# Optimization experiments

Measured on AMD Instinct MI355X. Metric: run time of the kernel, lower is better.

Reference implementation:

```python
import jax, jax.numpy as jnp
import numpy as np

NUM_ROWS = 16384
H = 2048
K = 4
EXPERT_NUM = 64


def setup_inputs() -> dict:
    key = jax.random.key(0)
    k1, k2, k3 = jax.random.split(key, 3)
    x = jax.random.normal(k1, (NUM_ROWS, H), dtype=jnp.float32)
    expert_idx = jax.random.randint(k2, (NUM_ROWS, K), 0, EXPERT_NUM, dtype=jnp.int32)
    scale = jax.random.uniform(k3, (NUM_ROWS,), dtype=jnp.float32)
    return {"x": x, "expert_idx": expert_idx, "scale": scale, "expert_num": EXPERT_NUM}


def reference(x, expert_idx, scale, expert_num):
    # Dropless MoE token routing (drop_pad_mode=0, active_num=0 -> all tokens,
    # quant_mode=-1 with scale, expert_tokens_num_type=1, full active range).
    num_rows, h = x.shape
    k = expert_idx.shape[-1]
    n = num_rows * k
    eidx = expert_idx.reshape(-1)                     # [n]
    sorted_idx = jnp.argsort(eidx, stable=True)       # stable sort by expert id
    src_row = sorted_idx // k                         # original token row per expanded slot
    expanded_x = x[src_row]                           # [n, h] gathered tokens, expert-grouped
    # inverse permutation: position of each original (row,k) slot in the expanded output
    expanded_row_idx = jnp.zeros((n,), dtype=jnp.int32).at[sorted_idx].set(
        jnp.arange(n, dtype=jnp.int32))
    expert_tokens_count = jnp.bincount(eidx, length=expert_num).astype(jnp.int32)
    expanded_scale = scale[src_row].astype(jnp.float32)  # [n]
    return expanded_x, expanded_row_idx, expert_tokens_count, expanded_scale
```

## Files before the change

### kernel.cpp

```cpp
#include <hip/hip_runtime.h>

#define NROWS   16384
#define HDIM    2048
#define TOPK    4
#define NEXP    64
#define NSLOT   (NROWS * TOPK)
#define SLOTS_PER_BLOCK 256
#define NBLK    (NSLOT / SLOTS_PER_BLOCK)
#define CHUNK   16
#define NCHUNK  (NBLK / CHUNK)

typedef float f4 __attribute__((ext_vector_type(4)));

__global__ void hist_rank_kernel(const int* __restrict__ eidx,
                                 int* __restrict__ hist,
                                 int* __restrict__ packed) {
    __shared__ int se[SLOTS_PER_BLOCK];
    __shared__ int h[NEXP];
    int t = threadIdx.x;
    if (t < NEXP) h[t] = 0;
    int slot = blockIdx.x * SLOTS_PER_BLOCK + t;
    int e = eidx[slot];
    se[t] = e;
    __syncthreads();
    int rank = 0, cnt = 0;
    #pragma unroll 8
    for (int i = 0; i < SLOTS_PER_BLOCK; ++i) {
        int m = (se[i] == e);
        cnt  += m;
        rank += (i < t) ? m : 0;
    }
    packed[slot] = (e << 16) | rank;
    if (rank == 0) h[e] = cnt;
    __syncthreads();
    if (t < NEXP) hist[blockIdx.x * NEXP + t] = h[t];
}

__global__ void __launch_bounds__(1024) scan_kernel(const int* __restrict__ hist,
                                                    int* __restrict__ base,
                                                    float* __restrict__ out_counts) {
    __shared__ int partial[NCHUNK][NEXP];
    __shared__ int expert_off[NEXP];
    int tid = threadIdx.x;
    int c = tid >> 6;
    int e = tid & 63;
    int b0 = c * CHUNK;

    int s = 0;
    #pragma unroll
    for (int i = 0; i < CHUNK; ++i) s += hist[(b0 + i) * NEXP + e];
    partial[c][e] = s;
    __syncthreads();

    int excl = 0;
    #pragma unroll
    for (int i = 0; i < NCHUNK; ++i) {
        int v = partial[i][e];
        excl += (i < c) ? v : 0;
    }

    if (tid < 64) {
        int total = 0;
        #pragma unroll
        for (int i = 0; i < NCHUNK; ++i) total += partial[i][tid];
        out_counts[tid] = (float)total;
        int incl = total;
        #pragma unroll
        for (int d = 1; d < 64; d <<= 1) {
            int y = __shfl_up(incl, d, 64);
            if (tid >= d) incl += y;
        }
        expert_off[tid] = incl - total;
    }
    __syncthreads();

    int running = expert_off[e] + excl;
    #pragma unroll
    for (int i = 0; i < CHUNK; ++i) {
        int idx = (b0 + i) * NEXP + e;
        base[idx] = running;
        running += hist[idx];
    }
}

__global__ void __launch_bounds__(256) copy_kernel(const f4* __restrict__ x,
                                                   const int* __restrict__ packed,
                                                   const int* __restrict__ base,
                                                   const float* __restrict__ scale,
                                                   float* __restrict__ out_idx,
                                                   float* __restrict__ out_scale,
                                                   f4* __restrict__ out) {
    int row = blockIdx.x;
    int t = threadIdx.x;
    const f4* xs = x + (size_t)row * (HDIM / 4);
    f4 v0 = __builtin_nontemporal_load(xs + t);
    f4 v1 = __builtin_nontemporal_load(xs + t + 256);

    int slot0 = row << 2;
    int b     = row >> 6;
    const int* bb = base + b * NEXP;
    int p0 = packed[slot0 + 0];
    int p1 = packed[slot0 + 1];
    int p2 = packed[slot0 + 2];
    int p3 = packed[slot0 + 3];
    int d0 = bb[p0 >> 16] + (p0 & 0xffff);
    int d1 = bb[p1 >> 16] + (p1 & 0xffff);
    int d2 = bb[p2 >> 16] + (p2 & 0xffff);
    int d3 = bb[p3 >> 16] + (p3 & 0xffff);

    if (t == 0) {
        f4 idx = {(float)d0, (float)d1, (float)d2, (float)d3};
        *reinterpret_cast<f4*>(out_idx + slot0) = idx;
        float sc = scale[row];
        out_scale[d0] = sc;
        out_scale[d1] = sc;
        out_scale[d2] = sc;
        out_scale[d3] = sc;
    }

    f4* o0 = out + (size_t)d0 * (HDIM / 4);
    f4* o1 = out + (size_t)d1 * (HDIM / 4);
    f4* o2 = out + (size_t)d2 * (HDIM / 4);
    f4* o3 = out + (size_t)d3 * (HDIM / 4);
    __builtin_nontemporal_store(v0, o0 + t);
    __builtin_nontemporal_store(v1, o0 + t + 256);
    __builtin_nontemporal_store(v0, o1 + t);
    __builtin_nontemporal_store(v1, o1 + t + 256);
    __builtin_nontemporal_store(v0, o2 + t);
    __builtin_nontemporal_store(v1, o2 + t + 256);
    __builtin_nontemporal_store(v0, o3 + t);
    __builtin_nontemporal_store(v1, o3 + t + 256);
}

extern "C" void kernel_launch(void* const* d_in, const int* in_sizes, int n_in,
                              void* d_out, int out_size, void* d_ws, size_t ws_size,
                              hipStream_t stream) {
    const float* x     = (const float*)d_in[0];
    const int*   eidx  = (const int*)d_in[1];
    const float* scale = (const float*)d_in[2];

    float* out        = (float*)d_out;
    float* out_x      = out;
    float* out_idx    = out + (size_t)NSLOT * HDIM;
    float* out_counts = out_idx + NSLOT;
    float* out_scale  = out_counts + NEXP;

    int* hist   = (int*)d_ws;
    int* base   = hist + NBLK * NEXP;
    int* packed = base + NBLK * NEXP;

    hist_rank_kernel<<<NBLK, SLOTS_PER_BLOCK, 0, stream>>>(eidx, hist, packed);
    scan_kernel<<<1, 1024, 0, stream>>>(hist, base, out_counts);
    copy_kernel<<<NROWS, 256, 0, stream>>>((const f4*)x, packed, base, scale,
                                           out_idx, out_scale, (f4*)out_x);
}
```

Measured before the change: 629.2 us.

## Fuse histogram and scan kernels via last-block atomic counter

Merges the per-block histogram/rank kernel and the single-block scan kernel into one launch. The last block to finish, found through an atomic counter and thread fences, performs the cross-block scan with 256 threads over larger chunks. This removes one kernel launch and its boundary, but adds a memset launch for the counter. The scan now runs serially on fewer threads with longer loops.

```diff
diff --git a/kernel.cpp b/kernel.cpp
--- a/kernel.cpp
+++ b/kernel.cpp
@@ -7,16 +7,18 @@
 #define NSLOT   (NROWS * TOPK)
 #define SLOTS_PER_BLOCK 256
 #define NBLK    (NSLOT / SLOTS_PER_BLOCK)
-#define CHUNK   16
-#define NCHUNK  (NBLK / CHUNK)
+#define SCHUNK  64
+#define NSCHUNK (NBLK / SCHUNK)
 
 typedef float f4 __attribute__((ext_vector_type(4)));
 
-__global__ void hist_rank_kernel(const int* __restrict__ eidx,
-                                 int* __restrict__ hist,
-                                 int* __restrict__ packed) {
+__global__ void __launch_bounds__(SLOTS_PER_BLOCK)
+meta_kernel(const int* __restrict__ eidx, int* __restrict__ hist,
+            int* __restrict__ base, int* __restrict__ packed,
+            int* __restrict__ counter, float* __restrict__ out_counts) {
     __shared__ int se[SLOTS_PER_BLOCK];
     __shared__ int h[NEXP];
+    __shared__ int is_last;
     int t = threadIdx.x;
     if (t < NEXP) h[t] = 0;
     int slot = blockIdx.x * SLOTS_PER_BLOCK + t;
@@ -34,50 +36,49 @@
     if (rank == 0) h[e] = cnt;
     __syncthreads();
     if (t < NEXP) hist[blockIdx.x * NEXP + t] = h[t];
-}
 
-__global__ void __launch_bounds__(1024) scan_kernel(const int* __restrict__ hist,
-                                                    int* __restrict__ base,
-                                                    float* __restrict__ out_counts) {
-    __shared__ int partial[NCHUNK][NEXP];
+    __threadfence();
+    if (t == 0) {
+        int prev = atomicAdd(counter, 1);
+        is_last = (prev == NBLK - 1);
+    }
+    __syncthreads();
+    if (!is_last) return;
+    __threadfence();
+
+    __shared__ int partial[NSCHUNK][NEXP];
     __shared__ int expert_off[NEXP];
-    int tid = threadIdx.x;
-    int c = tid >> 6;
-    int e = tid & 63;
-    int b0 = c * CHUNK;
+    int c  = t >> 6;
+    int ee = t & 63;
+    int b0 = c * SCHUNK;
 
     int s = 0;
-    #pragma unroll
-    for (int i = 0; i < CHUNK; ++i) s += hist[(b0 + i) * NEXP + e];
-    partial[c][e] = s;
+    for (int i = 0; i < SCHUNK; ++i) s += hist[(b0 + i) * NEXP + ee];
+    partial[c][ee] = s;
     __syncthreads();
 
     int excl = 0;
     #pragma unroll
-    for (int i = 0; i < NCHUNK; ++i) {
-        int v = partial[i][e];
-        excl += (i < c) ? v : 0;
-    }
+    for (int i = 0; i < NSCHUNK; ++i) excl += (i < c) ? partial[i][ee] : 0;
 
-    if (tid < 64) {
+    if (t < 64) {
         int total = 0;
         #pragma unroll
-        for (int i = 0; i < NCHUNK; ++i) total += partial[i][tid];
-        out_counts[tid] = (float)total;
+        for (int i = 0; i < NSCHUNK; ++i) total += partial[i][t];
+        out_counts[t] = (float)total;
         int incl = total;
         #pragma unroll
         for (int d = 1; d < 64; d <<= 1) {
             int y = __shfl_up(incl, d, 64);
-            if (tid >= d) incl += y;
+            if (t >= d) incl += y;
         }
-        expert_off[tid] = incl - total;
+        expert_off[t] = incl - total;
     }
     __syncthreads();
 
-    int running = expert_off[e] + excl;
-    #pragma unroll
-    for (int i = 0; i < CHUNK; ++i) {
-        int idx = (b0 + i) * NEXP + e;
+    int running = expert_off[ee] + excl;
+    for (int i = 0; i < SCHUNK; ++i) {
+        int idx = (b0 + i) * NEXP + ee;
         base[idx] = running;
         running += hist[idx];
     }
@@ -145,12 +146,15 @@
     float* out_counts = out_idx + NSLOT;
     float* out_scale  = out_counts + NEXP;
 
-    int* hist   = (int*)d_ws;
-    int* base   = hist + NBLK * NEXP;
-    int* packed = base + NBLK * NEXP;
+    int* hist    = (int*)d_ws;
+    int* base    = hist + NBLK * NEXP;
+    int* packed  = base + NBLK * NEXP;
+    int* counter = packed + NSLOT;
 
-    hist_rank_kernel<<<NBLK, SLOTS_PER_BLOCK, 0, stream>>>(eidx, hist, packed);
-    scan_kernel<<<1, 1024, 0, stream>>>(hist, base, out_counts);
+    hipMemsetAsync(counter, 0, sizeof(int), stream);
+
+    meta_kernel<<<NBLK, SLOTS_PER_BLOCK, 0, stream>>>(eidx, hist, base, packed,
+                                                      counter, out_counts);
     copy_kernel<<<NROWS, 256, 0, stream>>>((const f4*)x, packed, base, scale,
                                            out_idx, out_scale, (f4*)out_x);
 }
```

Result: slower. 648.1 us (+3.0%).
